# Kernel optimization log

Hardware: AMD Instinct MI355X
Metric: run time of the kernel (lower is better)

The kernel has to match this reference:

```python
import jax, jax.numpy as jnp
import numpy as np

D_MODEL = 1024
NHEAD = 16
D_FF = 4 * D_MODEL
EPS = 1e-5


def layer_norm(x, gamma, beta):
    mu = jnp.mean(x, axis=-1, keepdims=True)
    var = jnp.mean(jnp.square(x - mu), axis=-1, keepdims=True)
    return (x - mu) * jax.lax.rsqrt(var + EPS) * gamma + beta


def setup_inputs() -> dict:
    key = jax.random.key(0)
    ks = jax.random.split(key, 12)
    B, S, D = 4, 2048, D_MODEL
    s = 1.0 / np.sqrt(D)
    return {
        "x": jax.random.normal(ks[0], (B, S, D), jnp.float32),
        "wq": jax.random.normal(ks[1], (D, D), jnp.float32) * s,
        "wk": jax.random.normal(ks[2], (D, D), jnp.float32) * s,
        "wv": jax.random.normal(ks[3], (D, D), jnp.float32) * s,
        "wo": jax.random.normal(ks[4], (D, D), jnp.float32) * s,
        "bo": jnp.zeros((D,), jnp.float32),
        "ln1_g": jnp.ones((D,), jnp.float32),
        "ln1_b": jnp.zeros((D,), jnp.float32),
        "ln2_g": jnp.ones((D,), jnp.float32),
        "ln2_b": jnp.zeros((D,), jnp.float32),
        "w1": jax.random.normal(ks[5], (D, D_FF), jnp.float32) * s,
        "b1": jnp.zeros((D_FF,), jnp.float32),
        "w2": jax.random.normal(ks[6], (D_FF, D), jnp.float32) * (1.0 / np.sqrt(D_FF)),
        "b2": jnp.zeros((D,), jnp.float32),
    }


def reference(x, wq, wk, wv, wo, bo, ln1_g, ln1_b, ln2_g, ln2_b, w1, b1, w2, b2):
    B, S, D = x.shape
    H = NHEAD
    Dh = D // H
    xn = layer_norm(x, ln1_g, ln1_b)
    # projections -> [B, H, S, Dh]
    q = jnp.einsum('bsd,de->bse', xn, wq).reshape(B, S, H, Dh).transpose(0, 2, 1, 3)
    k = jnp.einsum('bsd,de->bse', xn, wk).reshape(B, S, H, Dh).transpose(0, 2, 1, 3)
    v = jnp.einsum('bsd,de->bse', xn, wv).reshape(B, S, H, Dh).transpose(0, 2, 1, 3)
    scores = jnp.einsum('bhsd,bhtd->bhst', q, k) / np.sqrt(Dh)  # [B,H,S,S]
    attn = jax.nn.softmax(scores, axis=-1)
    ctx = jnp.einsum('bhst,bhtd->bhsd', attn, v)
    ctx = ctx.transpose(0, 2, 1, 3).reshape(B, S, D)
    att_out = jnp.einsum('bsd,de->bse', ctx, wo) + bo
    xt = x + att_out
    h = layer_norm(xt, ln2_g, ln2_b)
    ffn = jnp.einsum('bsf,fd->bsd', jax.nn.relu(jnp.einsum('bsd,df->bsf', h, w1) + b1), w2) + b2
    return xt + ffn
```

## Files before the change

kernel.cpp:

```cpp
#include <hip/hip_runtime.h>
#include <stdint.h>

typedef __attribute__((ext_vector_type(8))) __bf16 bf16x8;
typedef __attribute__((ext_vector_type(4))) __bf16 bf16x4;
typedef __attribute__((ext_vector_type(4))) float f32x4;
typedef unsigned short u16;

#define D_MODEL 1024
#define D_FF 4096
#define SEQ 2048
#define NHEAD 16
#define DH 64
#define MROWS 8192

__device__ __forceinline__ u16 f2bf(float f) {
  union { float f; unsigned u; } v; v.f = f;
  unsigned r = v.u + 0x7fffu + ((v.u >> 16) & 1u);
  return (u16)(r >> 16);
}

__device__ __forceinline__ void gload16(const u16* g, u16* l) {
  __builtin_amdgcn_global_load_lds((const __attribute__((address_space(1))) void*)(g),
                                   (__attribute__((address_space(3))) void*)(l),
                                   16, 0, 0);
}

__device__ __forceinline__ void block_bar() {
  asm volatile("" ::: "memory");
  __builtin_amdgcn_s_barrier();
  asm volatile("" ::: "memory");
}

template <int N>
__device__ __forceinline__ void wait_vm() {
  if constexpr (N == 6)      asm volatile("s_waitcnt vmcnt(6)" ::: "memory");
  else if constexpr (N == 4) asm volatile("s_waitcnt vmcnt(4)" ::: "memory");
  else if constexpr (N == 3) asm volatile("s_waitcnt vmcnt(3)" ::: "memory");
  else                       asm volatile("s_waitcnt vmcnt(0)" ::: "memory");
}

__global__ __launch_bounds__(256)
void wconv_kernel(const float* __restrict__ W, u16* __restrict__ Wt, int K, int N,
                  float scale) {
  __shared__ u16 t[32][33];
  const int tid = threadIdx.x, tx = tid & 31, ty = tid >> 5;
  const int n0 = blockIdx.x * 32, k0 = blockIdx.y * 32;
#pragma unroll
  for (int i = 0; i < 4; ++i) {
    int k = ty + i * 8;
    t[k][tx] = f2bf(W[(size_t)(k0 + k) * N + n0 + tx] * scale);
  }
  __syncthreads();
#pragma unroll
  for (int i = 0; i < 4; ++i) {
    int n = ty + i * 8;
    Wt[(size_t)(n0 + n) * K + k0 + tx] = t[tx][n];
  }
}

__global__ __launch_bounds__(256)
void ln_kernel(const float* __restrict__ x, u16* __restrict__ out,
               const float* __restrict__ g, const float* __restrict__ beta) {
  const int row = blockIdx.x, tid = threadIdx.x;
  const float4 v = reinterpret_cast<const float4*>(x + (size_t)row * D_MODEL)[tid];
  float s = v.x + v.y + v.z + v.w;
#pragma unroll
  for (int off = 32; off; off >>= 1) s += __shfl_down(s, off);
  __shared__ float red[8];
  if ((tid & 63) == 0) red[tid >> 6] = s;
  __syncthreads();
  const float mu = (red[0] + red[1] + red[2] + red[3]) * (1.0f / D_MODEL);
  const float dx = v.x - mu, dy = v.y - mu, dz = v.z - mu, dw = v.w - mu;
  float sq = dx * dx + dy * dy + dz * dz + dw * dw;
#pragma unroll
  for (int off = 32; off; off >>= 1) sq += __shfl_down(sq, off);
  if ((tid & 63) == 0) red[4 + (tid >> 6)] = sq;
  __syncthreads();
  const float var = (red[4] + red[5] + red[6] + red[7]) * (1.0f / D_MODEL);
  const float rs = rsqrtf(var + 1e-5f);
  const float4 gv = reinterpret_cast<const float4*>(g)[tid];
  const float4 bv = reinterpret_cast<const float4*>(beta)[tid];
  ushort4 ov;
  ov.x = f2bf(dx * rs * gv.x + bv.x);
  ov.y = f2bf(dy * rs * gv.y + bv.y);
  ov.z = f2bf(dz * rs * gv.z + bv.z);
  ov.w = f2bf(dw * rs * gv.w + bv.w);
  reinterpret_cast<ushort4*>(out + (size_t)row * D_MODEL)[tid] = ov;
}

template <int BM, int EPI>
__global__ __launch_bounds__(512, 2)
void gemm8p_kernel(const u16* __restrict__ A, const u16* __restrict__ Bt,
                   int N, int K,
                   const float* __restrict__ bias,
                   const float* __restrict__ res,
                   float* __restrict__ outf, u16* __restrict__ outb,
                   u16* __restrict__ outb2, u16* __restrict__ outb3) {
  constexpr int WM = BM / 2;
  constexpr int MREP = WM / 16;
  constexpr int MI = 2;
  constexpr int ACH = BM / 64;
  constexpr int VN = (BM == 256) ? 6 : 3;
  __shared__ __align__(16) u16 Al[2][BM * 64];
  __shared__ __align__(16) u16 Bl[2][256 * 64];
  const int tid = threadIdx.x, lane = tid & 63, wave = tid >> 6;
  const int wr = wave >> 2, wc = wave & 3;
  const int l16 = lane & 15, g8 = lane >> 4;
  const int srw = lane >> 3;
  const int scl = ((lane & 7) ^ (lane >> 3)) * 8;
  const int swz = (l16 & 7) << 3;
  const int mBase = blockIdx.y * BM, nBase = blockIdx.x * 256;
  const int nt = K >> 6;

  f32x4 acc[MREP][4];
#pragma unroll
  for (int mi = 0; mi < MREP; ++mi)
#pragma unroll
    for (int nj = 0; nj < 4; ++nj) acc[mi][nj] = f32x4{0.f, 0.f, 0.f, 0.f};

  auto stageChunk = [&](int tile, int c) {
    if (tile >= nt) return;
    const int buf = tile & 1;
    if (c < ACH) {
      const int r0 = c * 64 + wave * 8;
      gload16(A + (size_t)(mBase + r0 + srw) * K + tile * 64 + scl,
              &Al[buf][r0 * 64]);
    } else {
      const int r0 = (c - ACH) * 64 + wave * 8;
      gload16(Bt + (size_t)(nBase + r0 + srw) * K + tile * 64 + scl,
              &Bl[buf][r0 * 64]);
    }
  };

  if constexpr (BM == 256) {
    constexpr int P0[8] = {4,5,6,7,0,2,1,3};
    constexpr int P1[6] = {4,5,6,7,0,2};
#pragma unroll
    for (int i = 0; i < 8; ++i) stageChunk(0, P0[i]);
#pragma unroll
    for (int i = 0; i < 6; ++i) stageChunk(1, P1[i]);
  } else {
    constexpr int P0[6] = {2,3,4,5,0,1};
    constexpr int P1[3] = {2,3,4};
#pragma unroll
    for (int i = 0; i < 6; ++i) stageChunk(0, P0[i]);
#pragma unroll
    for (int i = 0; i < 3; ++i) stageChunk(1, P1[i]);
  }
  wait_vm<VN>();
  block_bar();

  if constexpr (BM == 256) {
    constexpr int STO[16] = {1,1, 2,2, 2,2, 2,2, 2,2, 3,3, 3,3, 3,3};
    constexpr int STC[16] = {1,3, 4,5, 6,7, 0,2, 1,3, 4,5, 6,7, 0,2};
    for (int T = 0; T < nt; T += 2) {
      bf16x8 bfr[4][2];
#pragma unroll
      for (int p = 0; p < 8; ++p) {
        const int q = p & 3;
        const int buf = p >> 2;
        if (q == 0) {
#pragma unroll
          for (int nj = 0; nj < 4; ++nj)
#pragma unroll
            for (int ks = 0; ks < 2; ++ks) {
              const int rb = wc * 64 + nj * 16 + l16;
              bfr[nj][ks] = *reinterpret_cast<const bf16x8*>(
                  &Bl[buf][rb * 64 + ((ks * 32 + g8 * 8) ^ swz)]);
            }
        }
        bf16x8 af[MI][2];
#pragma unroll
        for (int i = 0; i < MI; ++i)
#pragma unroll
          for (int ks = 0; ks < 2; ++ks) {
            const int ra = wr * WM + (q * MI + i) * 16 + l16;
            af[i][ks] = *reinterpret_cast<const bf16x8*>(
                &Al[buf][ra * 64 + ((ks * 32 + g8 * 8) ^ swz)]);
          }
        stageChunk(T + STO[2 * p], STC[2 * p]);
        stageChunk(T + STO[2 * p + 1], STC[2 * p + 1]);
        block_bar();
        __builtin_amdgcn_s_setprio(1);
#pragma unroll
        for (int i = 0; i < MI; ++i)
#pragma unroll
          for (int nj = 0; nj < 4; ++nj)
#pragma unroll
            for (int ks = 0; ks < 2; ++ks)
              acc[q * MI + i][nj] = __builtin_amdgcn_mfma_f32_16x16x32_bf16(
                  af[i][ks], bfr[nj][ks], acc[q * MI + i][nj], 0, 0, 0);
        __builtin_amdgcn_s_setprio(0);
        if (p == 3) {
          if (T + 2 < nt) wait_vm<VN>(); else wait_vm<0>();
        } else if (p == 7) {
          wait_vm<VN>();
        }
        block_bar();
      }
    }
  } else {
    constexpr int STO[12] = {1,1,1, 2,2,2, 2,2,2, 3,3,3};
    constexpr int STC[12] = {5,0,1, 2,3,4, 5,0,1, 2,3,4};
    for (int T = 0; T < nt; T += 2) {
      bf16x8 bfr[4][2];
#pragma unroll
      for (int p = 0; p < 4; ++p) {
        const int q = p & 1;
        const int buf = p >> 1;
        if (q == 0) {
#pragma unroll
          for (int nj = 0; nj < 4; ++nj)
#pragma unroll
            for (int ks = 0; ks < 2; ++ks) {
              const int rb = wc * 64 + nj * 16 + l16;
              bfr[nj][ks] = *reinterpret_cast<const bf16x8*>(
                  &Bl[buf][rb * 64 + ((ks * 32 + g8 * 8) ^ swz)]);
            }
        }
        bf16x8 af[MI][2];
#pragma unroll
        for (int i = 0; i < MI; ++i)
#pragma unroll
          for (int ks = 0; ks < 2; ++ks) {
            const int ra = wr * WM + (q * MI + i) * 16 + l16;
            af[i][ks] = *reinterpret_cast<const bf16x8*>(
                &Al[buf][ra * 64 + ((ks * 32 + g8 * 8) ^ swz)]);
          }
        stageChunk(T + STO[3 * p], STC[3 * p]);
        stageChunk(T + STO[3 * p + 1], STC[3 * p + 1]);
        stageChunk(T + STO[3 * p + 2], STC[3 * p + 2]);
        block_bar();
        __builtin_amdgcn_s_setprio(1);
#pragma unroll
        for (int i = 0; i < MI; ++i)
#pragma unroll
          for (int nj = 0; nj < 4; ++nj)
#pragma unroll
            for (int ks = 0; ks < 2; ++ks)
              acc[q * MI + i][nj] = __builtin_amdgcn_mfma_f32_16x16x32_bf16(
                  af[i][ks], bfr[nj][ks], acc[q * MI + i][nj], 0, 0, 0);
        __builtin_amdgcn_s_setprio(0);
        if (p == 1) {
          if (T + 2 < nt) wait_vm<VN>(); else wait_vm<0>();
        } else if (p == 3) {
          if (T + 3 < nt) wait_vm<VN>(); else wait_vm<0>();
        }
        block_bar();
      }
    }
  }

#pragma unroll
  for (int mi = 0; mi < MREP; ++mi)
#pragma unroll
    for (int nj = 0; nj < 4; ++nj) {
      const int colB = wc * 64 + nj * 16 + l16;
      const int row0 = mBase + wr * WM + mi * 16 + g8 * 4;
      if (EPI == 4) {
        const int seg = nBase >> 10;
        const int c = (nBase & 1023) + colB;
        if (seg == 2) {
          const int bi = row0 >> 11, s = row0 & 2047;
          ushort4 pk;
          pk.x = f2bf(acc[mi][nj][0]);
          pk.y = f2bf(acc[mi][nj][1]);
          pk.z = f2bf(acc[mi][nj][2]);
          pk.w = f2bf(acc[mi][nj][3]);
          *reinterpret_cast<ushort4*>(outb3 + ((size_t)(bi << 10) + c) * SEQ + s) = pk;
        } else {
          u16* o = (seg == 0) ? outb : outb2;
#pragma unroll
          for (int r = 0; r < 4; ++r)
            o[(size_t)(row0 + r) * D_MODEL + c] = f2bf(acc[mi][nj][r]);
        }
      } else {
        const int col = nBase + colB;
        const float bv = bias[col];
#pragma unroll
        for (int r = 0; r < 4; ++r) {
          const size_t idx = (size_t)(row0 + r) * N + col;
          const float vv = acc[mi][nj][r];
          if (EPI == 1) {
            outf[idx] = vv + bv + res[idx];
          } else {
            const float tv = vv + bv;
            outb[idx] = f2bf(tv > 0.f ? tv : 0.f);
          }
        }
      }
    }
}

__global__ __launch_bounds__(256)
void attn_kernel(const u16* __restrict__ qb, const u16* __restrict__ kb,
                 const u16* __restrict__ vb, u16* __restrict__ ctx) {
  __shared__ __align__(16) u16 Kl[2][64 * 64];
  __shared__ __align__(16) u16 Vl[2][64 * 64];
  __shared__ __align__(16) u16 Pl[4][32 * 64];
  const int tid = threadIdx.x;
  const int lane = tid & 63, wave = tid >> 6, g8 = lane >> 4, l16 = lane & 15;
  const int b = blockIdx.y >> 4, h = blockIdx.y & 15;
  const int q0 = blockIdx.x * 128 + wave * 32;
  const size_t rowB = (size_t)b * SEQ;
  const int colH = h * DH;
  const size_t vtBase = (size_t)(b * 1024 + colH) * SEQ;
  const int srw = lane >> 3;
  const int scl = ((lane & 7) ^ (lane >> 3)) * 8;
  const int cswz = (l16 & 7) * 8;

  bf16x8 qf[2][2];
#pragma unroll
  for (int m = 0; m < 2; ++m)
#pragma unroll
    for (int ks = 0; ks < 2; ++ks)
      qf[m][ks] = *reinterpret_cast<const bf16x8*>(
          qb + (rowB + q0 + m * 16 + l16) * D_MODEL + colH + ks * 32 + g8 * 8);

  float mi[2] = {-1e30f, -1e30f}, li[2] = {0.f, 0.f};
  f32x4 o[2][4];
#pragma unroll
  for (int m = 0; m < 2; ++m)
#pragma unroll
    for (int nt = 0; nt < 4; ++nt) o[m][nt] = f32x4{0.f, 0.f, 0.f, 0.f};

  auto stageKV = [&](int t0, int buf) {
    if (t0 >= SEQ) return;
#pragma unroll
    for (int i = 0; i < 2; ++i) {
      const int r0 = wave * 16 + i * 8;
      gload16(kb + (rowB + t0 + r0 + srw) * D_MODEL + colH + scl, &Kl[buf][r0 * 64]);
      gload16(vb + vtBase + (size_t)(r0 + srw) * SEQ + t0 + scl, &Vl[buf][r0 * 64]);
    }
  };

  stageKV(0, 0);
  wait_vm<0>();
  block_bar();

  int buf = 0;
  for (int t0 = 0; t0 < SEQ; t0 += 64, buf ^= 1) {
    stageKV(t0 + 64, buf ^ 1);

    f32x4 st[2][4];
#pragma unroll
    for (int m = 0; m < 2; ++m)
#pragma unroll
      for (int kt = 0; kt < 4; ++kt) st[m][kt] = f32x4{0.f, 0.f, 0.f, 0.f};
#pragma unroll
    for (int kt = 0; kt < 4; ++kt) {
      const bf16x8 kf0 = *reinterpret_cast<const bf16x8*>(
          &Kl[buf][(kt * 16 + l16) * 64 + ((g8 * 8) ^ cswz)]);
      const bf16x8 kf1 = *reinterpret_cast<const bf16x8*>(
          &Kl[buf][(kt * 16 + l16) * 64 + ((32 + g8 * 8) ^ cswz)]);
#pragma unroll
      for (int m = 0; m < 2; ++m) {
        st[m][kt] = __builtin_amdgcn_mfma_f32_16x16x32_bf16(kf0, qf[m][0], st[m][kt], 0, 0, 0);
        st[m][kt] = __builtin_amdgcn_mfma_f32_16x16x32_bf16(kf1, qf[m][1], st[m][kt], 0, 0, 0);
      }
    }

    float alpha[2];
    bool dor[2];
#pragma unroll
    for (int m = 0; m < 2; ++m) {
      float pmax = st[m][0][0];
#pragma unroll
      for (int kt = 0; kt < 4; ++kt)
#pragma unroll
        for (int r = 0; r < 4; ++r) pmax = fmaxf(pmax, st[m][kt][r]);
      pmax = fmaxf(pmax, __shfl_xor(pmax, 16));
      pmax = fmaxf(pmax, __shfl_xor(pmax, 32));
      dor[m] = !__all(pmax - mi[m] <= 8.0f);
      alpha[m] = 1.0f;
      if (dor[m]) {
        const float mnew = fmaxf(mi[m], pmax);
        alpha[m] = __builtin_amdgcn_exp2f(mi[m] - mnew);
        mi[m] = mnew;
      }
      float sum = 0.f;
#pragma unroll
      for (int kt = 0; kt < 4; ++kt) {
        bf16x4 pk;
#pragma unroll
        for (int r = 0; r < 4; ++r) {
          const float p = __builtin_amdgcn_exp2f(st[m][kt][r] - mi[m]);
          sum += p;
          pk[r] = (__bf16)p;
        }
        const int row = m * 16 + l16;
        *reinterpret_cast<bf16x4*>(
            &Pl[wave][row * 64 + ((kt * 16 + g8 * 4) ^ cswz)]) = pk;
      }
      sum += __shfl_xor(sum, 16);
      sum += __shfl_xor(sum, 32);
      li[m] = li[m] * alpha[m] + sum;
    }

#pragma unroll
    for (int m = 0; m < 2; ++m) {
      if (dor[m]) {
        f32x4 al;
#pragma unroll
        for (int r = 0; r < 4; ++r) al[r] = __shfl(alpha[m], g8 * 4 + r);
#pragma unroll
        for (int nt = 0; nt < 4; ++nt) {
          f32x4 t = o[m][nt];
          t[0] *= al[0]; t[1] *= al[1]; t[2] *= al[2]; t[3] *= al[3];
          o[m][nt] = t;
        }
      }
    }

    bf16x8 pf[2][2];
#pragma unroll
    for (int m = 0; m < 2; ++m)
#pragma unroll
      for (int ks = 0; ks < 2; ++ks)
        pf[m][ks] = *reinterpret_cast<const bf16x8*>(
            &Pl[wave][(m * 16 + l16) * 64 + ((ks * 32 + g8 * 8) ^ cswz)]);
#pragma unroll
    for (int nt = 0; nt < 4; ++nt) {
      const bf16x8 vf0 = *reinterpret_cast<const bf16x8*>(
          &Vl[buf][(nt * 16 + l16) * 64 + ((g8 * 8) ^ cswz)]);
      const bf16x8 vf1 = *reinterpret_cast<const bf16x8*>(
          &Vl[buf][(nt * 16 + l16) * 64 + ((32 + g8 * 8) ^ cswz)]);
#pragma unroll
      for (int m = 0; m < 2; ++m) {
        o[m][nt] = __builtin_amdgcn_mfma_f32_16x16x32_bf16(pf[m][0], vf0, o[m][nt], 0, 0, 0);
        o[m][nt] = __builtin_amdgcn_mfma_f32_16x16x32_bf16(pf[m][1], vf1, o[m][nt], 0, 0, 0);
      }
    }

    wait_vm<0>();
    block_bar();
  }

#pragma unroll
  for (int m = 0; m < 2; ++m) {
    f32x4 ld;
#pragma unroll
    for (int r = 0; r < 4; ++r) ld[r] = 1.0f / __shfl(li[m], g8 * 4 + r);
#pragma unroll
    for (int nt = 0; nt < 4; ++nt)
#pragma unroll
      for (int r = 0; r < 4; ++r) {
        const __bf16 v = (__bf16)(o[m][nt][r] * ld[r]);
        ctx[(rowB + q0 + m * 16 + g8 * 4 + r) * D_MODEL + colH + nt * 16 + l16] =
            __builtin_bit_cast(u16, v);
      }
  }
}

extern "C" void kernel_launch(void* const* d_in, const int* in_sizes, int n_in,
                              void* d_out, int out_size, void* d_ws, size_t ws_size,
                              hipStream_t stream) {
  const float* x   = (const float*)d_in[0];
  const float* wq  = (const float*)d_in[1];
  const float* wk  = (const float*)d_in[2];
  const float* wv  = (const float*)d_in[3];
  const float* wo  = (const float*)d_in[4];
  const float* bo  = (const float*)d_in[5];
  const float* l1g = (const float*)d_in[6];
  const float* l1b = (const float*)d_in[7];
  const float* l2g = (const float*)d_in[8];
  const float* l2b = (const float*)d_in[9];
  const float* w1  = (const float*)d_in[10];
  const float* b1  = (const float*)d_in[11];
  const float* w2  = (const float*)d_in[12];
  const float* b2  = (const float*)d_in[13];
  float* outp = (float*)d_out;

  uint8_t* ws = (uint8_t*)d_ws;
  const size_t MB = 1024 * 1024;
  u16* wqkvt = (u16*)(ws + 0 * MB);
  u16* wqt   = wqkvt;
  u16* wkt   = (u16*)(ws + 2 * MB);
  u16* wvt   = (u16*)(ws + 4 * MB);
  u16* wot   = (u16*)(ws + 6 * MB);
  u16* w1t   = (u16*)(ws + 8 * MB);
  u16* w2t   = (u16*)(ws + 16 * MB);
  u16* xn    = (u16*)(ws + 24 * MB);
  u16* qbuf  = (u16*)(ws + 40 * MB);
  u16* kbuf  = (u16*)(ws + 56 * MB);
  u16* vbufT = (u16*)(ws + 72 * MB);
  u16* ctx   = xn;
  u16* hbuf  = qbuf;
  u16* ffh   = kbuf;

  dim3 blk(256);
  dim3 blk5(512);

  wconv_kernel<<<dim3(32, 32), blk, 0, stream>>>(wq, wqt, 1024, 1024, 0.18033688011112042f);
  wconv_kernel<<<dim3(32, 32), blk, 0, stream>>>(wk, wkt, 1024, 1024, 1.0f);
  wconv_kernel<<<dim3(32, 32), blk, 0, stream>>>(wv, wvt, 1024, 1024, 1.0f);
  wconv_kernel<<<dim3(32, 32), blk, 0, stream>>>(wo, wot, 1024, 1024, 1.0f);
  wconv_kernel<<<dim3(128, 32), blk, 0, stream>>>(w1, w1t, 1024, 4096, 1.0f);
  wconv_kernel<<<dim3(32, 128), blk, 0, stream>>>(w2, w2t, 4096, 1024, 1.0f);

  ln_kernel<<<MROWS, blk, 0, stream>>>(x, xn, l1g, l1b);

  gemm8p_kernel<128, 4><<<dim3(12, 64), blk5, 0, stream>>>(
      xn, wqkvt, 3072, 1024, nullptr, nullptr, nullptr, qbuf, kbuf, vbufT);

  attn_kernel<<<dim3(16, 64), blk, 0, stream>>>(qbuf, kbuf, vbufT, ctx);

  gemm8p_kernel<128, 1><<<dim3(4, 64), blk5, 0, stream>>>(
      ctx, wot, 1024, 1024, bo, x, outp, nullptr, nullptr, nullptr);

  ln_kernel<<<MROWS, blk, 0, stream>>>(outp, hbuf, l2g, l2b);

  gemm8p_kernel<256, 2><<<dim3(16, 32), blk5, 0, stream>>>(
      hbuf, w1t, 4096, 1024, b1, nullptr, nullptr, ffh, nullptr, nullptr);

  gemm8p_kernel<128, 1><<<dim3(4, 64), blk5, 0, stream>>>(
      ffh, w2t, 1024, 4096, b2, outp, outp, nullptr, nullptr, nullptr);
}
```

Measured before the change: 548.2 us.

## Replace 128x256 GEMM path with 4-wave 128x128 tile kernel for QKV, Wo, W2

```diff
diff --git a/kernel.cpp b/kernel.cpp
--- a/kernel.cpp
+++ b/kernel.cpp
@@ -35,7 +35,7 @@
 __device__ __forceinline__ void wait_vm() {
   if constexpr (N == 6)      asm volatile("s_waitcnt vmcnt(6)" ::: "memory");
   else if constexpr (N == 4) asm volatile("s_waitcnt vmcnt(4)" ::: "memory");
-  else if constexpr (N == 3) asm volatile("s_waitcnt vmcnt(3)" ::: "memory");
+  else if constexpr (N == 2) asm volatile("s_waitcnt vmcnt(2)" ::: "memory");
   else                       asm volatile("s_waitcnt vmcnt(0)" ::: "memory");
 }
 
@@ -98,9 +98,9 @@
                    u16* __restrict__ outb2, u16* __restrict__ outb3) {
   constexpr int WM = BM / 2;
   constexpr int MREP = WM / 16;
-  constexpr int MI = 2;
+  constexpr int MI = MREP / 4;
   constexpr int ACH = BM / 64;
-  constexpr int VN = (BM == 256) ? 6 : 3;
+  constexpr int VN = 6;
   __shared__ __align__(16) u16 Al[2][BM * 64];
   __shared__ __align__(16) u16 Bl[2][256 * 64];
   const int tid = threadIdx.x, lane = tid & 63, wave = tid >> 6;
@@ -132,122 +132,61 @@
     }
   };
 
-  if constexpr (BM == 256) {
-    constexpr int P0[8] = {4,5,6,7,0,2,1,3};
-    constexpr int P1[6] = {4,5,6,7,0,2};
-#pragma unroll
-    for (int i = 0; i < 8; ++i) stageChunk(0, P0[i]);
-#pragma unroll
-    for (int i = 0; i < 6; ++i) stageChunk(1, P1[i]);
-  } else {
-    constexpr int P0[6] = {2,3,4,5,0,1};
-    constexpr int P1[3] = {2,3,4};
-#pragma unroll
-    for (int i = 0; i < 6; ++i) stageChunk(0, P0[i]);
-#pragma unroll
-    for (int i = 0; i < 3; ++i) stageChunk(1, P1[i]);
-  }
+  constexpr int STO256[16] = {1,1, 2,2, 2,2, 2,2, 2,2, 3,3, 3,3, 3,3};
+  constexpr int STC256[16] = {1,3, 4,5, 6,7, 0,2, 1,3, 4,5, 6,7, 0,2};
+  constexpr int P0_256[8] = {4,5,6,7,0,2,1,3};
+  constexpr int P1_256[6] = {4,5,6,7,0,2};
+#pragma unroll
+  for (int i = 0; i < 8; ++i) stageChunk(0, P0_256[i]);
+#pragma unroll
+  for (int i = 0; i < 6; ++i) stageChunk(1, P1_256[i]);
   wait_vm<VN>();
   block_bar();
 
-  if constexpr (BM == 256) {
-    constexpr int STO[16] = {1,1, 2,2, 2,2, 2,2, 2,2, 3,3, 3,3, 3,3};
-    constexpr int STC[16] = {1,3, 4,5, 6,7, 0,2, 1,3, 4,5, 6,7, 0,2};
-    for (int T = 0; T < nt; T += 2) {
-      bf16x8 bfr[4][2];
-#pragma unroll
-      for (int p = 0; p < 8; ++p) {
-        const int q = p & 3;
-        const int buf = p >> 2;
-        if (q == 0) {
-#pragma unroll
-          for (int nj = 0; nj < 4; ++nj)
-#pragma unroll
-            for (int ks = 0; ks < 2; ++ks) {
-              const int rb = wc * 64 + nj * 16 + l16;
-              bfr[nj][ks] = *reinterpret_cast<const bf16x8*>(
-                  &Bl[buf][rb * 64 + ((ks * 32 + g8 * 8) ^ swz)]);
-            }
+  for (int T = 0; T < nt; T += 2) {
+    bf16x8 bfr[4][2];
+#pragma unroll
+    for (int p = 0; p < 8; ++p) {
+      const int q = p & 3;
+      const int buf = p >> 2;
+      if (q == 0) {
+#pragma unroll
+        for (int nj = 0; nj < 4; ++nj)
+#pragma unroll
+          for (int ks = 0; ks < 2; ++ks) {
+            const int rb = wc * 64 + nj * 16 + l16;
+            bfr[nj][ks] = *reinterpret_cast<const bf16x8*>(
+                &Bl[buf][rb * 64 + ((ks * 32 + g8 * 8) ^ swz)]);
+          }
+      }
+      bf16x8 af[MI][2];
+#pragma unroll
+      for (int i = 0; i < MI; ++i)
+#pragma unroll
+        for (int ks = 0; ks < 2; ++ks) {
+          const int ra = wr * WM + (q * MI + i) * 16 + l16;
+          af[i][ks] = *reinterpret_cast<const bf16x8*>(
+              &Al[buf][ra * 64 + ((ks * 32 + g8 * 8) ^ swz)]);
         }
-        bf16x8 af[MI][2];
-#pragma unroll
-        for (int i = 0; i < MI; ++i)
-#pragma unroll
-          for (int ks = 0; ks < 2; ++ks) {
-            const int ra = wr * WM + (q * MI + i) * 16 + l16;
-            af[i][ks] = *reinterpret_cast<const bf16x8*>(
-                &Al[buf][ra * 64 + ((ks * 32 + g8 * 8) ^ swz)]);
-          }
-        stageChunk(T + STO[2 * p], STC[2 * p]);
-        stageChunk(T + STO[2 * p + 1], STC[2 * p + 1]);
-        block_bar();
-        __builtin_amdgcn_s_setprio(1);
-#pragma unroll
-        for (int i = 0; i < MI; ++i)
-#pragma unroll
-          for (int nj = 0; nj < 4; ++nj)
-#pragma unroll
-            for (int ks = 0; ks < 2; ++ks)
-              acc[q * MI + i][nj] = __builtin_amdgcn_mfma_f32_16x16x32_bf16(
-                  af[i][ks], bfr[nj][ks], acc[q * MI + i][nj], 0, 0, 0);
-        __builtin_amdgcn_s_setprio(0);
-        if (p == 3) {
-          if (T + 2 < nt) wait_vm<VN>(); else wait_vm<0>();
-        } else if (p == 7) {
-          wait_vm<VN>();
-        }
-        block_bar();
-      }
-    }
-  } else {
-    constexpr int STO[12] = {1,1,1, 2,2,2, 2,2,2, 3,3,3};
-    constexpr int STC[12] = {5,0,1, 2,3,4, 5,0,1, 2,3,4};
-    for (int T = 0; T < nt; T += 2) {
-      bf16x8 bfr[4][2];
-#pragma unroll
-      for (int p = 0; p < 4; ++p) {
-        const int q = p & 1;
-        const int buf = p >> 1;
-        if (q == 0) {
-#pragma unroll
-          for (int nj = 0; nj < 4; ++nj)
-#pragma unroll
-            for (int ks = 0; ks < 2; ++ks) {
-              const int rb = wc * 64 + nj * 16 + l16;
-              bfr[nj][ks] = *reinterpret_cast<const bf16x8*>(
-                  &Bl[buf][rb * 64 + ((ks * 32 + g8 * 8) ^ swz)]);
-            }
-        }
-        bf16x8 af[MI][2];
-#pragma unroll
-        for (int i = 0; i < MI; ++i)
-#pragma unroll
-          for (int ks = 0; ks < 2; ++ks) {
-            const int ra = wr * WM + (q * MI + i) * 16 + l16;
-            af[i][ks] = *reinterpret_cast<const bf16x8*>(
-                &Al[buf][ra * 64 + ((ks * 32 + g8 * 8) ^ swz)]);
-          }
-        stageChunk(T + STO[3 * p], STC[3 * p]);
-        stageChunk(T + STO[3 * p + 1], STC[3 * p + 1]);
-        stageChunk(T + STO[3 * p + 2], STC[3 * p + 2]);
-        block_bar();
-        __builtin_amdgcn_s_setprio(1);
-#pragma unroll
-        for (int i = 0; i < MI; ++i)
-#pragma unroll
-          for (int nj = 0; nj < 4; ++nj)
-#pragma unroll
-            for (int ks = 0; ks < 2; ++ks)
-              acc[q * MI + i][nj] = __builtin_amdgcn_mfma_f32_16x16x32_bf16(
-                  af[i][ks], bfr[nj][ks], acc[q * MI + i][nj], 0, 0, 0);
-        __builtin_amdgcn_s_setprio(0);
-        if (p == 1) {
-          if (T + 2 < nt) wait_vm<VN>(); else wait_vm<0>();
-        } else if (p == 3) {
-          if (T + 3 < nt) wait_vm<VN>(); else wait_vm<0>();
-        }
-        block_bar();
-      }
+      stageChunk(T + STO256[2 * p], STC256[2 * p]);
+      stageChunk(T + STO256[2 * p + 1], STC256[2 * p + 1]);
+      block_bar();
+      __builtin_amdgcn_s_setprio(1);
+#pragma unroll
+      for (int i = 0; i < MI; ++i)
+#pragma unroll
+        for (int nj = 0; nj < 4; ++nj)
+#pragma unroll
+          for (int ks = 0; ks < 2; ++ks)
+            acc[q * MI + i][nj] = __builtin_amdgcn_mfma_f32_16x16x32_bf16(
+                af[i][ks], bfr[nj][ks], acc[q * MI + i][nj], 0, 0, 0);
+      __builtin_amdgcn_s_setprio(0);
+      if (p == 3) {
+        if (T + 2 < nt) wait_vm<VN>(); else wait_vm<0>();
+      } else if (p == 7) {
+        wait_vm<VN>();
+      }
+      block_bar();
     }
   }
 
@@ -257,6 +196,128 @@
     for (int nj = 0; nj < 4; ++nj) {
       const int colB = wc * 64 + nj * 16 + l16;
       const int row0 = mBase + wr * WM + mi * 16 + g8 * 4;
+      const int col = nBase + colB;
+      const float bv = bias[col];
+#pragma unroll
+      for (int r = 0; r < 4; ++r) {
+        const size_t idx = (size_t)(row0 + r) * N + col;
+        const float vv = acc[mi][nj][r];
+        if (EPI == 1) {
+          outf[idx] = vv + bv + res[idx];
+        } else {
+          const float tv = vv + bv;
+          outb[idx] = f2bf(tv > 0.f ? tv : 0.f);
+        }
+      }
+    }
+}
+
+template <int EPI>
+__global__ __launch_bounds__(256, 2)
+void gemm4w_kernel(const u16* __restrict__ A, const u16* __restrict__ Bt,
+                   int N, int K,
+                   const float* __restrict__ bias,
+                   const float* __restrict__ res,
+                   float* __restrict__ outf, u16* __restrict__ outb,
+                   u16* __restrict__ outb2, u16* __restrict__ outb3) {
+  __shared__ __align__(16) u16 Al[2][128 * 64];
+  __shared__ __align__(16) u16 Bl[2][128 * 64];
+  const int tid = threadIdx.x, lane = tid & 63, wave = tid >> 6;
+  const int wr = wave >> 1, wc = wave & 1;
+  const int l16 = lane & 15, g8 = lane >> 4;
+  const int srw = lane >> 3;
+  const int scl = ((lane & 7) ^ (lane >> 3)) * 8;
+  const int swz = (l16 & 7) << 3;
+  const int mBase = blockIdx.y * 128, nBase = blockIdx.x * 128;
+  const int nt = K >> 6;
+
+  f32x4 acc[4][4];
+#pragma unroll
+  for (int mi = 0; mi < 4; ++mi)
+#pragma unroll
+    for (int nj = 0; nj < 4; ++nj) acc[mi][nj] = f32x4{0.f, 0.f, 0.f, 0.f};
+
+  auto stage2A = [&](int tile, int q0) {
+    if (tile >= nt) return;
+    const int b = tile & 1;
+#pragma unroll
+    for (int qq = 0; qq < 2; ++qq) {
+      const int row0 = ((wave & 2) ? 64 : 0) + (q0 + qq) * 16 + (wave & 1) * 8;
+      gload16(A + (size_t)(mBase + row0 + srw) * K + tile * 64 + scl,
+              &Al[b][row0 * 64]);
+    }
+  };
+  auto stage2B = [&](int tile, int b0) {
+    if (tile >= nt) return;
+    const int b = tile & 1;
+#pragma unroll
+    for (int bb = 0; bb < 2; ++bb) {
+      const int row0 = (b0 + bb) * 32 + wave * 8;
+      gload16(Bt + (size_t)(nBase + row0 + srw) * K + tile * 64 + scl,
+              &Bl[b][row0 * 64]);
+    }
+  };
+
+  stage2B(0, 0); stage2B(0, 2); stage2A(0, 0); stage2A(0, 2);
+  wait_vm<2>();
+  block_bar();
+
+  for (int T = 0; T < nt; T += 2) {
+    bf16x8 bfr[4][2];
+#pragma unroll
+    for (int p = 0; p < 8; ++p) {
+      const int q = p & 3;
+      const int buf = p >> 2;
+      const int tO = T + 1 + buf;
+      if (q == 0) {
+#pragma unroll
+        for (int nj = 0; nj < 4; ++nj)
+#pragma unroll
+          for (int ks = 0; ks < 2; ++ks) {
+            const int rb = wc * 64 + nj * 16 + l16;
+            bfr[nj][ks] = *reinterpret_cast<const bf16x8*>(
+                &Bl[buf][rb * 64 + ((ks * 32 + g8 * 8) ^ swz)]);
+          }
+      }
+      bf16x8 af[2];
+#pragma unroll
+      for (int ks = 0; ks < 2; ++ks) {
+        const int ra = wr * 64 + q * 16 + l16;
+        af[ks] = *reinterpret_cast<const bf16x8*>(
+            &Al[buf][ra * 64 + ((ks * 32 + g8 * 8) ^ swz)]);
+      }
+      if (q == 0)      stage2B(tO, 0);
+      else if (q == 1) stage2B(tO, 2);
+      else if (q == 2) stage2A(tO, 0);
+      else             stage2A(tO, 2);
+      block_bar();
+      __builtin_amdgcn_s_setprio(1);
+#pragma unroll
+      for (int nj = 0; nj < 4; ++nj)
+#pragma unroll
+        for (int ks = 0; ks < 2; ++ks)
+          acc[q][nj] = __builtin_amdgcn_mfma_f32_16x16x32_bf16(
+              af[ks], bfr[nj][ks], acc[q][nj], 0, 0, 0);
+      __builtin_amdgcn_s_setprio(0);
+      if (p == 1) {
+        wait_vm<4>();
+      } else if (p == 3) {
+        wait_vm<2>();
+      } else if (p == 5) {
+        if (T + 2 < nt) wait_vm<4>(); else wait_vm<0>();
+      } else if (p == 7) {
+        if (T + 2 < nt) wait_vm<2>(); else wait_vm<0>();
+      }
+      block_bar();
+    }
+  }
+
+#pragma unroll
+  for (int mi = 0; mi < 4; ++mi)
+#pragma unroll
+    for (int nj = 0; nj < 4; ++nj) {
+      const int colB = wc * 64 + nj * 16 + l16;
+      const int row0 = mBase + wr * 64 + mi * 16 + g8 * 4;
       if (EPI == 4) {
         const int seg = nBase >> 10;
         const int c = (nBase & 1023) + colB;
@@ -280,13 +341,7 @@
 #pragma unroll
         for (int r = 0; r < 4; ++r) {
           const size_t idx = (size_t)(row0 + r) * N + col;
-          const float vv = acc[mi][nj][r];
-          if (EPI == 1) {
-            outf[idx] = vv + bv + res[idx];
-          } else {
-            const float tv = vv + bv;
-            outb[idx] = f2bf(tv > 0.f ? tv : 0.f);
-          }
+          outf[idx] = acc[mi][nj][r] + bv + res[idx];
         }
       }
     }
@@ -500,12 +555,12 @@
 
   ln_kernel<<<MROWS, blk, 0, stream>>>(x, xn, l1g, l1b);
 
-  gemm8p_kernel<128, 4><<<dim3(12, 64), blk5, 0, stream>>>(
+  gemm4w_kernel<4><<<dim3(24, 64), blk, 0, stream>>>(
       xn, wqkvt, 3072, 1024, nullptr, nullptr, nullptr, qbuf, kbuf, vbufT);
 
   attn_kernel<<<dim3(16, 64), blk, 0, stream>>>(qbuf, kbuf, vbufT, ctx);
 
-  gemm8p_kernel<128, 1><<<dim3(4, 64), blk5, 0, stream>>>(
+  gemm4w_kernel<1><<<dim3(8, 64), blk, 0, stream>>>(
       ctx, wot, 1024, 1024, bo, x, outp, nullptr, nullptr, nullptr);
 
   ln_kernel<<<MROWS, blk, 0, stream>>>(outp, hbuf, l2g, l2b);
@@ -513,6 +568,6 @@
   gemm8p_kernel<256, 2><<<dim3(16, 32), blk5, 0, stream>>>(
       hbuf, w1t, 4096, 1024, b1, nullptr, nullptr, ffh, nullptr, nullptr);
 
-  gemm8p_kernel<128, 1><<<dim3(4, 64), blk5, 0, stream>>>(
+  gemm4w_kernel<1><<<dim3(8, 64), blk, 0, stream>>>(
       ffh, w2t, 1024, 4096, b2, outp, outp, nullptr, nullptr, nullptr);
 }
```

Result: no change. 538.2 us (-1.8%).
